# Kernel optimization log

Hardware: AMD Instinct MI355X
Metric: run time of the kernel (lower is better)

The kernel has to match this reference:

```python
import jax, jax.numpy as jnp
import numpy as np

N = 16384
D_IN = 64
D_HID = D_IN // 2  # 32
D_OUT = 32


def setup_inputs() -> dict:
    key = jax.random.key(0)
    kA, kX, k1, k2, k3 = jax.random.split(key, 5)
    # Dense adjacency-like operator [N, N]; scaled so activations stay sane.
    A = jax.random.normal(kA, (N, N), dtype=jnp.float32) / np.sqrt(N)
    X = jax.random.normal(kX, (N, D_IN), dtype=jnp.float32)
    # torch nn.Linear weights: [out_features, in_features], no bias
    W1 = jax.random.normal(k1, (D_IN, D_IN), dtype=jnp.float32) / np.sqrt(D_IN)
    W2 = jax.random.normal(k2, (D_HID, D_IN), dtype=jnp.float32) / np.sqrt(D_IN)
    W3 = jax.random.normal(k3, (D_OUT, D_HID), dtype=jnp.float32) / np.sqrt(D_HID)
    return {"A": A, "X": X, "W1": W1, "W2": W2, "W3": W3}


def reference(A, X, W1, W2, W3):
    # Layer 1: relu(fc1(A @ X)); fc(x) = x @ W.T
    h = jax.nn.relu((A @ X) @ W1.T)        # [N, D_IN]
    # Layer 2: relu(fc2(A @ h))
    h = jax.nn.relu((A @ h) @ W2.T)        # [N, D_HID]
    # Layer 3: fc3(A @ h), no activation
    return (A @ h) @ W3.T                  # [N, D_OUT]
```

## Files before the change

kernel.cpp:

```cpp
#include <hip/hip_runtime.h>
#include <cstdint>
#include <cstddef>


#define NN 16384
#define SK1 8
#define KC1 (NN / SK1)
#define SK2 16
#define KC2 (NN / SK2)
#define NKB (NN / 32)

typedef __attribute__((ext_vector_type(8))) short s16x8;
typedef __attribute__((ext_vector_type(4))) float fx4;

__device__ __forceinline__ unsigned short f2bf_rne(float f) {
    unsigned int x = __builtin_bit_cast(unsigned int, f);
    x += 0x7fffu + ((x >> 16) & 1u);
    return (unsigned short)(x >> 16);
}

__device__ __forceinline__ s16x8 pack_bf(fx4 a, fx4 b) {
    s16x8 t;
    t[0] = (short)f2bf_rne(a[0]);
    t[1] = (short)f2bf_rne(a[1]);
    t[2] = (short)f2bf_rne(a[2]);
    t[3] = (short)f2bf_rne(a[3]);
    t[4] = (short)f2bf_rne(b[0]);
    t[5] = (short)f2bf_rne(b[1]);
    t[6] = (short)f2bf_rne(b[2]);
    t[7] = (short)f2bf_rne(b[3]);
    return t;
}

template <int SAVE>
__global__ __launch_bounds__(256, 4) void k_spmm1(
    const float* __restrict__ A32,
    unsigned short* __restrict__ Abf,
    const unsigned short* __restrict__ PT,
    float* __restrict__ part)
{
    const int lane = threadIdx.x & 63;
    const int wv   = threadIdx.x >> 6;
    const int srow = lane & 15;
    const int kg   = lane >> 4;
    const int s    = blockIdx.y;
    const long kbeg = (long)s * KC1;
    const int rowbase = blockIdx.x * 128 + wv * 32;
    const long r0 = rowbase + srow;
    const long r1 = rowbase + 16 + srow;
    const long g0 = rowbase >> 4, g1 = g0 + 1;

    fx4 acc0[4], acc1[4];
#pragma unroll
    for (int c = 0; c < 4; ++c) {
        acc0[c] = (fx4){0.f, 0.f, 0.f, 0.f};
        acc1[c] = (fx4){0.f, 0.f, 0.f, 0.f};
    }

#pragma unroll 2
    for (int i = 0; i < KC1 / 32; ++i) {
        const long ko = kbeg + (long)i * 32;
        const long kblk = ko >> 5;
        const float* p0 = A32 + r0 * (long)NN + ko + kg * 4;
        const float* p1 = A32 + r1 * (long)NN + ko + kg * 4;
        fx4 a00 = __builtin_nontemporal_load((const fx4*)p0);
        fx4 a01 = __builtin_nontemporal_load((const fx4*)(p0 + 16));
        fx4 a10 = __builtin_nontemporal_load((const fx4*)p1);
        fx4 a11 = __builtin_nontemporal_load((const fx4*)(p1 + 16));
        s16x8 af0 = pack_bf(a00, a01);
        s16x8 af1 = pack_bf(a10, a11);
        if (SAVE) {
            *(s16x8*)(Abf + ((g0 * NKB + kblk) * 64 + lane) * 8) = af0;
            *(s16x8*)(Abf + ((g1 * NKB + kblk) * 64 + lane) * 8) = af1;
        }
#pragma unroll
        for (int c = 0; c < 4; ++c) {
            s16x8 bf = *(const s16x8*)(PT + (long)(c * 16 + srow) * NN + ko + kg * 8);
            acc0[c] = __builtin_amdgcn_mfma_f32_16x16x32_bf16(af0, bf, acc0[c], 0, 0, 0);
            acc1[c] = __builtin_amdgcn_mfma_f32_16x16x32_bf16(af1, bf, acc1[c], 0, 0, 0);
        }
    }
    float* pbase = part + (long)s * NN * 64;
#pragma unroll
    for (int c = 0; c < 4; ++c)
#pragma unroll
        for (int r = 0; r < 4; ++r) {
            pbase[(long)(rowbase + kg * 4 + r) * 64 + c * 16 + srow]      = acc0[c][r];
            pbase[(long)(rowbase + 16 + kg * 4 + r) * 64 + c * 16 + srow] = acc1[c][r];
        }
}

template <int ABF>
__global__ __launch_bounds__(256, 4) void k_spmm2(
    const unsigned short* __restrict__ Abf,
    const float* __restrict__ A32,
    const unsigned short* __restrict__ PT,
    float* __restrict__ part)
{
    const int lane = threadIdx.x & 63;
    const int wv   = threadIdx.x >> 6;
    const int srow = lane & 15;
    const int kg   = lane >> 4;
    const int s    = blockIdx.y;
    const long kbeg = (long)s * KC2;
    const int rowbase = blockIdx.x * 256 + wv * 64;
    const long g0 = rowbase >> 4;

    fx4 acc[4][2];
#pragma unroll
    for (int t = 0; t < 4; ++t)
#pragma unroll
        for (int c = 0; c < 2; ++c) acc[t][c] = (fx4){0.f, 0.f, 0.f, 0.f};

#pragma unroll 2
    for (int i = 0; i < KC2 / 32; ++i) {
        const long ko = kbeg + (long)i * 32;
        const long kblk = ko >> 5;
        s16x8 af[4];
        if (ABF) {
#pragma unroll
            for (int t = 0; t < 4; ++t)
                af[t] = *(const s16x8*)(Abf + (((g0 + t) * NKB + kblk) * 64 + lane) * 8);
        } else {
#pragma unroll
            for (int t = 0; t < 4; ++t) {
                const float* p = A32 + (long)(rowbase + t * 16 + srow) * NN + ko + kg * 4;
                fx4 a0 = __builtin_nontemporal_load((const fx4*)p);
                fx4 a1 = __builtin_nontemporal_load((const fx4*)(p + 16));
                af[t] = pack_bf(a0, a1);
            }
        }
        s16x8 b0 = *(const s16x8*)(PT + (long)srow * NN + ko + kg * 8);
        s16x8 b1 = *(const s16x8*)(PT + (long)(16 + srow) * NN + ko + kg * 8);
#pragma unroll
        for (int t = 0; t < 4; ++t) {
            acc[t][0] = __builtin_amdgcn_mfma_f32_16x16x32_bf16(af[t], b0, acc[t][0], 0, 0, 0);
            acc[t][1] = __builtin_amdgcn_mfma_f32_16x16x32_bf16(af[t], b1, acc[t][1], 0, 0, 0);
        }
    }
    float* pbase = part + (long)s * NN * 32;
#pragma unroll
    for (int t = 0; t < 4; ++t)
#pragma unroll
        for (int c = 0; c < 2; ++c)
#pragma unroll
            for (int r = 0; r < 4; ++r)
                pbase[(long)(rowbase + t * 16 + kg * 4 + r) * 32 + c * 16 + srow] = acc[t][c][r];
}

template <int DIN, int DOUT, int NSUM, bool RELU>
__global__ __launch_bounds__(256) void k_proj(
    const float* __restrict__ src,
    const float* __restrict__ W,
    unsigned short* __restrict__ PT)
{
    __shared__ float Ws[DOUT * DIN];
    __shared__ float Hs[64][DIN + 1];
    const int tid = threadIdx.x;
    for (int i = tid; i < DOUT * DIN; i += 256) Ws[i] = W[i];
    const int rbase = blockIdx.x * 64;
    for (int i = tid; i < 64 * DIN; i += 256) {
        const int rl = i / DIN, k = i % DIN;
        float v = 0.f;
#pragma unroll
        for (int s2 = 0; s2 < NSUM; ++s2)
            v += src[(long)s2 * NN * DIN + (long)(rbase + rl) * DIN + k];
        Hs[rl][k] = RELU ? fmaxf(v, 0.f) : v;
    }
    __syncthreads();
    const int rl = tid & 63;
    const int c0 = tid >> 6;
    const int r  = rbase + rl;
    const int kk = r & 31;
    const int pidx = (r & ~31) + ((kk & 15) >> 2) * 8 + (kk & 3) + ((kk >> 4) << 2);
    for (int c = c0; c < DOUT; c += 4) {
        float accv = 0.f;
#pragma unroll
        for (int k = 0; k < DIN; ++k) accv += Hs[rl][k] * Ws[c * DIN + k];
        PT[(long)c * NN + pidx] = f2bf_rne(accv);
    }
}

__global__ __launch_bounds__(256) void k_red(
    const float* __restrict__ part, float* __restrict__ out)
{
    const int e = blockIdx.x * 256 + threadIdx.x;
    if (e >= NN * 32 / 4) return;
    fx4 v = (fx4){0.f, 0.f, 0.f, 0.f};
#pragma unroll
    for (int s = 0; s < SK2; ++s)
        v += *(const fx4*)(part + (long)s * NN * 32 + (long)e * 4);
    *(fx4*)(out + (long)e * 4) = v;
}

extern "C" void kernel_launch(void* const* d_in, const int* in_sizes, int n_in,
                              void* d_out, int out_size, void* d_ws, size_t ws_size,
                              hipStream_t stream) {
    const float* A  = (const float*)d_in[0];
    const float* X  = (const float*)d_in[1];
    const float* W1 = (const float*)d_in[2];
    const float* W2 = (const float*)d_in[3];
    const float* W3 = (const float*)d_in[4];
    float* out = (float*)d_out;

    char* ws = (char*)d_ws;
    const size_t part_b = (size_t)SK1 * NN * 64 * 4;
    const size_t pt_b   = (size_t)64 * NN * 2;
    const size_t abf_b  = (size_t)NN * NN * 2;
    float*          part = (float*)ws;
    unsigned short* PT   = (unsigned short*)(ws + part_b);
    unsigned short* Abf  = (unsigned short*)(ws + part_b + pt_b);
    const bool save = ws_size >= part_b + pt_b + abf_b;

    dim3 b(256);
    dim3 gP(NN / 64);
    dim3 g1(NN / 128, SK1);
    dim3 g2(NN / 256, SK2);

    k_proj<64, 64, 1, false><<<gP, b, 0, stream>>>(X, W1, PT);
    if (save) k_spmm1<1><<<g1, b, 0, stream>>>(A, Abf, PT, part);
    else      k_spmm1<0><<<g1, b, 0, stream>>>(A, Abf, PT, part);

    k_proj<64, 32, SK1, true><<<gP, b, 0, stream>>>(part, W2, PT);
    if (save) k_spmm2<1><<<g2, b, 0, stream>>>(Abf, A, PT, part);
    else      k_spmm2<0><<<g2, b, 0, stream>>>(Abf, A, PT, part);

    k_proj<32, 32, SK2, true><<<gP, b, 0, stream>>>(part, W3, PT);
    if (save) k_spmm2<1><<<g2, b, 0, stream>>>(Abf, A, PT, part);
    else      k_spmm2<0><<<g2, b, 0, stream>>>(Abf, A, PT, part);

    k_red<<<dim3(NN * 32 / 4 / 256), b, 0, stream>>>(part, out);
}
```

Measured before the change: 689.5 us.

## Stage A tiles through swizzled LDS with coalesced loads in first SpMM

The first A-times-P kernel is restructured so each block handles 16 rows with 4 waves splitting the 64 output columns. Contiguous row segments of fp32 A are loaded with coalesced 16-byte loads, converted to bf16 and written into a double-buffered XOR-swizzled LDS tile. The MFMA fragments and the saved bf16 copy of A are then read from that tile. This removes the strided 16-row gather of the old per-lane fragment loads, but adds LDS traffic, barriers, and 8x more blocks that each read the P operand separately.

Result: no change. 699.9 us (+1.5%).

```diff
diff --git a/kernel.cpp b/kernel.cpp
--- a/kernel.cpp
+++ b/kernel.cpp
@@ -6,6 +6,8 @@
 #define NN 16384
 #define SK1 8
 #define KC1 (NN / SK1)
+#define CH 512
+#define NCH (KC1 / CH)
 #define SK2 16
 #define KC2 (NN / SK2)
 #define NKB (NN / 32)
@@ -39,55 +41,80 @@
     const unsigned short* __restrict__ PT,
     float* __restrict__ part)
 {
-    const int lane = threadIdx.x & 63;
-    const int wv   = threadIdx.x >> 6;
-    const int srow = lane & 15;
-    const int kg   = lane >> 4;
-    const int s    = blockIdx.y;
+    __shared__ unsigned short Asm[2][16 * 512];
+    const int tid  = threadIdx.x;
+    const int lane = tid & 63, wv = tid >> 6;
+    const int srow = lane & 15, kg = lane >> 4;
+    const int s  = blockIdx.y;
+    const int gR = blockIdx.x;
+    const long R = (long)gR * 16;
     const long kbeg = (long)s * KC1;
-    const int rowbase = blockIdx.x * 128 + wv * 32;
-    const long r0 = rowbase + srow;
-    const long r1 = rowbase + 16 + srow;
-    const long g0 = rowbase >> 4, g1 = g0 + 1;
-
-    fx4 acc0[4], acc1[4];
-#pragma unroll
-    for (int c = 0; c < 4; ++c) {
-        acc0[c] = (fx4){0.f, 0.f, 0.f, 0.f};
-        acc1[c] = (fx4){0.f, 0.f, 0.f, 0.f};
-    }
-
-#pragma unroll 2
-    for (int i = 0; i < KC1 / 32; ++i) {
-        const long ko = kbeg + (long)i * 32;
-        const long kblk = ko >> 5;
-        const float* p0 = A32 + r0 * (long)NN + ko + kg * 4;
-        const float* p1 = A32 + r1 * (long)NN + ko + kg * 4;
-        fx4 a00 = __builtin_nontemporal_load((const fx4*)p0);
-        fx4 a01 = __builtin_nontemporal_load((const fx4*)(p0 + 16));
-        fx4 a10 = __builtin_nontemporal_load((const fx4*)p1);
-        fx4 a11 = __builtin_nontemporal_load((const fx4*)(p1 + 16));
-        s16x8 af0 = pack_bf(a00, a01);
-        s16x8 af1 = pack_bf(a10, a11);
+
+    fx4 acc = (fx4){0.f, 0.f, 0.f, 0.f};
+    fx4 gld[8];
+
+    auto LOADG = [&](int c) {
+#pragma unroll
+        for (int j = 0; j < 8; ++j) {
+            const int u = wv * 8 + j;
+            const int r = u >> 1, seg = u & 1;
+            const float* p = A32 + (R + r) * (long)NN + kbeg + (long)c * CH
+                             + seg * 256 + lane * 4;
+            gld[j] = __builtin_nontemporal_load((const fx4*)p);
+        }
+    };
+    auto STORE_LDS = [&](int buf) {
+#pragma unroll
+        for (int j = 0; j < 8; ++j) {
+            const int u = wv * 8 + j;
+            const int r = u >> 1, seg = u & 1;
+            const int kt = seg * 256 + lane * 4;
+            const int kblk = kt >> 5;
+            const int kb   = kt & 31;
+            const int flane = (r & 15) + (((kb & 15) >> 2) << 4);
+            const int half  = kb >> 4;
+            uint2 v;
+            v.x = (unsigned)f2bf_rne(gld[j][0]) | ((unsigned)f2bf_rne(gld[j][1]) << 16);
+            v.y = (unsigned)f2bf_rne(gld[j][2]) | ((unsigned)f2bf_rne(gld[j][3]) << 16);
+            const int boff = kblk * 1024 + ((flane * 16 + half * 8) ^ ((kblk & 7) << 4));
+            *(uint2*)((char*)&Asm[buf][0] + boff) = v;
+        }
+    };
+    auto COMPUTE = [&](int buf, int c) {
+#pragma unroll
+        for (int ks = 0; ks < 16; ++ks) {
+            const int aoff = ks * 1024 + ((lane * 16) ^ ((ks & 7) << 4));
+            s16x8 af = *(const s16x8*)((const char*)&Asm[buf][0] + aoff);
+            s16x8 bf = *(const s16x8*)(PT + (long)(wv * 16 + srow) * NN + kbeg
+                                       + (long)c * CH + ks * 32 + kg * 8);
+            acc = __builtin_amdgcn_mfma_f32_16x16x32_bf16(af, bf, acc, 0, 0, 0);
+        }
         if (SAVE) {
-            *(s16x8*)(Abf + ((g0 * NKB + kblk) * 64 + lane) * 8) = af0;
-            *(s16x8*)(Abf + ((g1 * NKB + kblk) * 64 + lane) * 8) = af1;
-        }
-#pragma unroll
-        for (int c = 0; c < 4; ++c) {
-            s16x8 bf = *(const s16x8*)(PT + (long)(c * 16 + srow) * NN + ko + kg * 8);
-            acc0[c] = __builtin_amdgcn_mfma_f32_16x16x32_bf16(af0, bf, acc0[c], 0, 0, 0);
-            acc1[c] = __builtin_amdgcn_mfma_f32_16x16x32_bf16(af1, bf, acc1[c], 0, 0, 0);
-        }
-    }
-    float* pbase = part + (long)s * NN * 64;
-#pragma unroll
-    for (int c = 0; c < 4; ++c)
-#pragma unroll
-        for (int r = 0; r < 4; ++r) {
-            pbase[(long)(rowbase + kg * 4 + r) * 64 + c * 16 + srow]      = acc0[c][r];
-            pbase[(long)(rowbase + 16 + kg * 4 + r) * 64 + c * 16 + srow] = acc1[c][r];
-        }
+            const long kb0 = (kbeg + (long)c * CH) >> 5;
+#pragma unroll
+            for (int t = 0; t < 4; ++t) {
+                const int kblk = wv * 4 + t;
+                const int aoff = kblk * 1024 + ((lane * 16) ^ ((kblk & 7) << 4));
+                s16x8 v = *(const s16x8*)((const char*)&Asm[buf][0] + aoff);
+                *(s16x8*)(Abf + (((long)gR * NKB + kb0 + kblk) * 64 + lane) * 8) = v;
+            }
+        }
+    };
+
+    LOADG(0);
+    STORE_LDS(0);
+    __syncthreads();
+    for (int c = 0; c < NCH; ++c) {
+        if (c + 1 < NCH) LOADG(c + 1);
+        COMPUTE(c & 1, c);
+        if (c + 1 < NCH) STORE_LDS((c + 1) & 1);
+        __syncthreads();
+    }
+
+    float* pb = part + (long)s * NN * 64 + R * 64;
+#pragma unroll
+    for (int r = 0; r < 4; ++r)
+        pb[(kg * 4 + r) * 64 + wv * 16 + srow] = acc[r];
 }
 
 template <int ABF>
@@ -214,7 +241,7 @@
 
     dim3 b(256);
     dim3 gP(NN / 64);
-    dim3 g1(NN / 128, SK1);
+    dim3 g1(NN / 16, SK1);
     dim3 g2(NN / 256, SK2);
 
     k_proj<64, 64, 1, false><<<gP, b, 0, stream>>>(X, W1, PT);
```
